# Optimization experiments

Hardware: AMD Instinct MI355X
Metric: run time of the kernel (lower is better)

## Reference

```python
import jax, jax.numpy as jnp
import numpy as np

B, T, E, H = 4, 1024, 1024, 16
D = E // H  # head_dim = 64


def setup_inputs() -> dict:
    key = jax.random.key(0)
    ks = jax.random.split(key, 6)
    s = 0.02  # realistic init scale for stable softmax
    return {
        "hidden_states": jax.random.normal(ks[0], (B, T, E), jnp.float32),
        "attention_mask": jnp.zeros((B, 1, T, T), jnp.float32),
        "Wq": jax.random.normal(ks[1], (E, E), jnp.float32) * s,
        "bq": jnp.zeros((E,), jnp.float32),
        "Wk": jax.random.normal(ks[2], (E, E), jnp.float32) * s,
        "bk": jnp.zeros((E,), jnp.float32),
        "Wv": jax.random.normal(ks[3], (E, E), jnp.float32) * s,
        "bv": jnp.zeros((E,), jnp.float32),
        "Wo": jax.random.normal(ks[4], (E, E), jnp.float32) * s,
        "bo": jnp.zeros((E,), jnp.float32),
    }


def reference(hidden_states, attention_mask, Wq, bq, Wk, bk, Wv, bv, Wo, bo):
    b, t, e = hidden_states.shape
    scaling = jnp.asarray(D, hidden_states.dtype) ** -0.5
    # q_proj weights/bias are pre-scaled in the module; equivalent to scaling q output
    q = (hidden_states @ Wq.T + bq) * scaling      # [B,T,E]
    k = hidden_states @ Wk.T + bk                   # self-attention path (no cache)
    v = hidden_states @ Wv.T + bv
    q = q.reshape(b, t, H, D)
    k = k.reshape(b, t, H, D)
    v = v.reshape(b, t, H, D)
    # bmm(q, k^T): [B,H,T,S] score matrix (materialized, as in the original)
    scores = jnp.einsum("bthd,bshd->bhts", q, k) + attention_mask
    probs = jax.nn.softmax(scores, axis=-1)
    ctx = jnp.einsum("bhts,bshd->bthd", probs, v).reshape(b, t, e)
    return ctx @ Wo.T + bo
```

## Files before the change

### kernel.cpp

```cpp
#include <hip/hip_runtime.h>
#include <math.h>

#define BB 4
#define TT 1024
#define EE 1024
#define HH 16
#define DD 64
#define KDIM 1024
#define N_HS (4096 * 1024)
#define N_W  (1024 * 1024)
#define NQKV (BB * HH * TT * DD)
#define LOG2E 1.44269504088896340736f

typedef _Float16 f16x8 __attribute__((ext_vector_type(8)));
typedef _Float16 f16x4 __attribute__((ext_vector_type(4)));
typedef _Float16 f16x2 __attribute__((ext_vector_type(2)));
typedef float    f32x4 __attribute__((ext_vector_type(4)));

__device__ __forceinline__ unsigned short f2h(float x) {
    _Float16 h = (_Float16)x;
    return __builtin_bit_cast(unsigned short, h);
}
__device__ __forceinline__ void split_h(float x, unsigned short& hi, unsigned short& lo) {
    _Float16 h = (_Float16)x;
    hi = __builtin_bit_cast(unsigned short, h);
    lo = f2h(x - (float)h);
}

__device__ __forceinline__ f16x2 cvt_pk(float a, float b) {
    return __builtin_bit_cast(f16x2, __builtin_amdgcn_cvt_pkrtz(a, b));
}

__device__ __forceinline__ void gload16(const void* g, void* l) {
    __builtin_amdgcn_global_load_lds(
        (const __attribute__((address_space(1))) void*)g,
        (__attribute__((address_space(3))) void*)l, 16, 0, 0);
}

__device__ __forceinline__ float mx3(float a, float b, float c) {
    return fmaxf(fmaxf(a, b), c);
}

__global__ __launch_bounds__(256)
void split_kernel(const float* __restrict__ hs,
                  const float* __restrict__ Wq, const float* __restrict__ Wk,
                  const float* __restrict__ Wv, const float* __restrict__ Wo,
                  const float* __restrict__ mask, int* __restrict__ mflag,
                  unsigned short* __restrict__ ws)
{
    const int u = blockIdx.x * 256 + threadIdx.x;
    if (u < (N_HS / 4) + N_W) {
        const float* src;
        unsigned short* dst;
        if (u < (N_HS / 4)) {
            src = hs + (size_t)u * 4;
            dst = ws + (size_t)u * 4;
        } else {
            int v = u - N_HS / 4;
            int wsel = v >> 18;
            int wo   = v & 0x3FFFF;
            const float* Wsrc = (wsel == 0) ? Wq : (wsel == 1) ? Wk : (wsel == 2) ? Wv : Wo;
            src = Wsrc + (size_t)wo * 4;
            dst = ws + (size_t)N_HS + (size_t)wsel * N_W + (size_t)wo * 4;
        }
        float4 x = *(const float4*)src;
        ushort4 h4;
        h4.x = f2h(x.x); h4.y = f2h(x.y); h4.z = f2h(x.z); h4.w = f2h(x.w);
        *(ushort4*)dst = h4;
    } else {
        int v = u - ((N_HS / 4) + N_W);
        float4 x = *(const float4*)(mask + (size_t)v * 4);
        bool nz = (x.x != 0.f) || (x.y != 0.f) || (x.z != 0.f) || (x.w != 0.f);
        if (__any(nz) && (threadIdx.x & 63) == 0)
            atomicOr(mflag, 1);
    }
}

__global__ __launch_bounds__(256)
void qkv_kernel(const unsigned short* __restrict__ hsp,
                const unsigned short* __restrict__ wqp,
                const float* __restrict__ bq, const float* __restrict__ bk,
                const float* __restrict__ bv,
                unsigned short* __restrict__ qkvb)
{
    __shared__ unsigned short Ah[128 * 64], Bh[128 * 64];

    const int widx  = blockIdx.x >> 3;
    const int nbase = (blockIdx.x & 7) * 128;
    const int mbase = blockIdx.y * 128;
    const unsigned short* Wp = wqp + (size_t)widx * N_W;
    const float* bias = (widx == 0) ? bq : (widx == 1) ? bk : bv;
    unsigned short* dst = qkvb + (size_t)widx * NQKV;
    const float scale = (widx == 0) ? 0.125f * LOG2E : 1.0f;

    const int tid  = threadIdx.x;
    const int w    = tid >> 6;
    const int lane = tid & 63;
    const int quad = lane >> 4;
    const int l16  = lane & 15;
    const int wm   = (w >> 1) * 64;
    const int wn   = (w & 1) * 64;

    f32x4 acc[4][4];
#pragma unroll
    for (int i = 0; i < 4; i++)
#pragma unroll
        for (int j = 0; j < 4; j++) acc[i][j] = (f32x4)0.f;

#pragma unroll 1
    for (int kt = 0; kt < KDIM; kt += 64) {
        __syncthreads();
#pragma unroll
        for (int i = 0; i < 4; i++) {
            int u = tid + i * 256;
            int r = u >> 3, cp = u & 7;
            int c = cp ^ (r & 7);
            gload16(hsp + (size_t)(mbase + r) * KDIM + kt + c * 8, &Ah[u * 8]);
            gload16(Wp  + (size_t)(nbase + r) * KDIM + kt + c * 8, &Bh[u * 8]);
        }
        __syncthreads();

#pragma unroll
        for (int ks = 0; ks < 2; ks++) {
            f16x8 af[4], bfr[4];
#pragma unroll
            for (int i = 0; i < 4; i++) {
                int r = wm + i * 16 + l16;
                af[i] = *(const f16x8*)&Ah[(r * 8 + ((ks * 4 + quad) ^ (r & 7))) * 8];
            }
#pragma unroll
            for (int j = 0; j < 4; j++) {
                int r = wn + j * 16 + l16;
                bfr[j] = *(const f16x8*)&Bh[(r * 8 + ((ks * 4 + quad) ^ (r & 7))) * 8];
            }
#pragma unroll
            for (int i = 0; i < 4; i++)
#pragma unroll
                for (int j = 0; j < 4; j++)
                    acc[i][j] = __builtin_amdgcn_mfma_f32_16x16x32_f16(af[i], bfr[j], acc[i][j], 0, 0, 0);
        }
    }

#pragma unroll
    for (int j = 0; j < 4; j++) {
        int n = nbase + wn + j * 16 + l16;
        int h = n >> 6, d = n & 63;
        float bj = bias[n];
#pragma unroll
        for (int i = 0; i < 4; i++)
#pragma unroll
            for (int rr = 0; rr < 4; rr++) {
                int m = mbase + wm + i * 16 + quad * 4 + rr;
                int b = m >> 10, t = m & 1023;
                dst[(((size_t)(b * HH + h) * TT + t) * DD + d)] =
                    f2h((acc[i][j][rr] + bj) * scale);
            }
    }
}

__global__ __launch_bounds__(256)
void vtrans_kernel(const unsigned short* __restrict__ vp,
                   unsigned short* __restrict__ vtp)
{
    __shared__ unsigned short Ts[64 * 72];
    const int bh = blockIdx.y;
    const int t0 = blockIdx.x * 64;
    const unsigned short* src = vp  + (size_t)bh * TT * DD + (size_t)t0 * DD;
    unsigned short*       dst = vtp + (size_t)bh * DD * TT + t0;
    const int tid = threadIdx.x;

#pragma unroll
    for (int i = 0; i < 2; i++) {
        int id = tid + i * 256;
        int r = id >> 3, c = id & 7;
        *(uint4*)&Ts[r * 72 + c * 8] = *(const uint4*)(src + (size_t)r * DD + c * 8);
    }
    __syncthreads();
#pragma unroll
    for (int i = 0; i < 2; i++) {
        int id = tid + i * 256;
        int d = id >> 3, c = id & 7;
        unsigned short tmp[8];
#pragma unroll
        for (int j = 0; j < 8; j++) tmp[j] = Ts[(c * 8 + j) * 72 + d];
        uint4 o;
        o.x = (unsigned int)tmp[0] | ((unsigned int)tmp[1] << 16);
        o.y = (unsigned int)tmp[2] | ((unsigned int)tmp[3] << 16);
        o.z = (unsigned int)tmp[4] | ((unsigned int)tmp[5] << 16);
        o.w = (unsigned int)tmp[6] | ((unsigned int)tmp[7] << 16);
        *(uint4*)(dst + (size_t)d * TT + c * 8) = o;
    }
}

__global__ __launch_bounds__(256)
void outproj_kernel(const unsigned short* __restrict__ ctxh,
                    const unsigned short* __restrict__ ctxl,
                    const unsigned short* __restrict__ wop,
                    const float* __restrict__ bo, float* __restrict__ out)
{
    __shared__ unsigned short Ach[64 * 64], Acl[64 * 64], Bh[128 * 64];

    const int nbase = blockIdx.x * 128;
    const int mbase = blockIdx.y * 64;

    const int tid  = threadIdx.x;
    const int w    = tid >> 6;
    const int lane = tid & 63;
    const int quad = lane >> 4;
    const int l16  = lane & 15;
    const int wm   = (w >> 1) * 32;
    const int wn   = (w & 1) * 64;

    f32x4 acc[2][4];
#pragma unroll
    for (int i = 0; i < 2; i++)
#pragma unroll
        for (int j = 0; j < 4; j++) acc[i][j] = (f32x4)0.f;

#pragma unroll 1
    for (int kt = 0; kt < KDIM; kt += 64) {
        __syncthreads();
#pragma unroll
        for (int i = 0; i < 2; i++) {
            int u = tid + i * 256;
            int r = u >> 3, cp = u & 7;
            int c = cp ^ (r & 7);
            size_t ga = (size_t)(mbase + r) * KDIM + kt + c * 8;
            gload16(ctxh + ga, &Ach[u * 8]);
            gload16(ctxl + ga, &Acl[u * 8]);
        }
#pragma unroll
        for (int i = 0; i < 4; i++) {
            int u = tid + i * 256;
            int r = u >> 3, cp = u & 7;
            int c = cp ^ (r & 7);
            gload16(wop + (size_t)(nbase + r) * KDIM + kt + c * 8, &Bh[u * 8]);
        }
        __syncthreads();

#pragma unroll
        for (int ks = 0; ks < 2; ks++) {
            f16x8 ah[2], al[2], bfr[4];
#pragma unroll
            for (int i = 0; i < 2; i++) {
                int r = wm + i * 16 + l16;
                int slot = (r * 8 + ((ks * 4 + quad) ^ (r & 7))) * 8;
                ah[i] = *(const f16x8*)&Ach[slot];
                al[i] = *(const f16x8*)&Acl[slot];
            }
#pragma unroll
            for (int j = 0; j < 4; j++) {
                int r = wn + j * 16 + l16;
                bfr[j] = *(const f16x8*)&Bh[(r * 8 + ((ks * 4 + quad) ^ (r & 7))) * 8];
            }
#pragma unroll
            for (int i = 0; i < 2; i++)
#pragma unroll
                for (int j = 0; j < 4; j++) {
                    acc[i][j] = __builtin_amdgcn_mfma_f32_16x16x32_f16(ah[i], bfr[j], acc[i][j], 0, 0, 0);
                    acc[i][j] = __builtin_amdgcn_mfma_f32_16x16x32_f16(al[i], bfr[j], acc[i][j], 0, 0, 0);
                }
        }
    }

#pragma unroll
    for (int j = 0; j < 4; j++) {
        int n = nbase + wn + j * 16 + l16;
        float bj = bo[n];
#pragma unroll
        for (int i = 0; i < 2; i++)
#pragma unroll
            for (int rr = 0; rr < 4; rr++) {
                int m = mbase + wm + i * 16 + quad * 4 + rr;
                out[(size_t)m * EE + n] = acc[i][j][rr] + bj;
            }
    }
}

__global__ __launch_bounds__(256)
void attn_kernel(const unsigned short* __restrict__ qp_, const unsigned short* __restrict__ kp_,
                 const unsigned short* __restrict__ vtp_,
                 const float* __restrict__ mask, const int* __restrict__ mflag,
                 unsigned short* __restrict__ ctxh, unsigned short* __restrict__ ctxl)
{
    __shared__ unsigned short Ks[2][64 * 64];
    __shared__ unsigned short Vt[2][64 * 64];

    const int orig = blockIdx.x;
    const int wgid = (orig & 7) * 64 + (orig >> 3);
    const int bh = wgid >> 3;
    const int b  = bh >> 4;
    const int h  = bh & 15;
    const int m0 = (wgid & 7) * 128;
    const size_t hoff = (size_t)bh * TT * DD;
    const unsigned short* qhp = qp_ + hoff;
    const unsigned short* khp = kp_ + hoff;
    const unsigned short* vtp = vtp_ + hoff;
    const float* mb = mask + (size_t)b * TT * TT;

    const int tid  = threadIdx.x;
    const int w    = tid >> 6;
    const int lane = tid & 63;
    const int quad = lane >> 4;
    const int l16  = lane & 15;
    const int mw   = m0 + w * 32;

    const int usemask = mflag[0];

    const int lm7 = l16 & 7;
    const int x0  = l16 * 64 + ((quad)     ^ lm7) * 8;
    const int x1  = l16 * 64 + ((4 + quad) ^ lm7) * 8;
    const int qh  = quad >> 1, ql = quad & 1;
    int yy[4];
#pragma unroll
    for (int t = 0; t < 4; t++)
        yy[t] = l16 * 64 + ((2 * t + qh) ^ lm7) * 8 + ql * 4;
    const unsigned short* Ksf = &Ks[0][0];
    const unsigned short* Vtf = &Vt[0][0];

    f16x8 qf[2][2];
#pragma unroll
    for (int g = 0; g < 2; g++)
#pragma unroll
        for (int s = 0; s < 2; s++)
            qf[g][s] = *(const f16x8*)(qhp + (size_t)(mw + g * 16 + l16) * DD + s * 32 + quad * 8);

    f32x4 o2[2][4];
#pragma unroll
    for (int g = 0; g < 2; g++)
#pragma unroll
        for (int u = 0; u < 4; u++) o2[g][u] = (f32x4)0.f;
    f32x4 lv[2];
    lv[0] = (f32x4)0.f; lv[1] = (f32x4)0.f;
    const f32x4 zc = (f32x4)0.f;
    f16x4 onesv;
    onesv[0] = (_Float16)1.f; onesv[1] = (_Float16)1.f;
    onesv[2] = (_Float16)1.f; onesv[3] = (_Float16)1.f;
    float m_i[2] = { -INFINITY, -INFINITY };

#pragma unroll
    for (int i = 0; i < 2; i++) {
        int u = tid + i * 256;
        int r = u >> 3, cp = u & 7;
        int c = cp ^ (r & 7);
        gload16(khp + (size_t)r * DD + c * 8, &Ks[0][u * 8]);
        gload16(vtp + (size_t)r * TT + c * 8, &Vt[0][u * 8]);
    }
    __syncthreads();

#pragma unroll 2
    for (int it = 0; it < 16; ++it) {
        const int n0  = it * 64;
        const int cur = it & 1;

        if (it < 15) {
#pragma unroll
            for (int i = 0; i < 2; i++) {
                int u = tid + i * 256;
                int r = u >> 3, cp = u & 7;
                int c = cp ^ (r & 7);
                gload16(khp + (size_t)(n0 + 64 + r) * DD + c * 8, &Ks[cur ^ 1][u * 8]);
                gload16(vtp + (size_t)r * TT + n0 + 64 + c * 8,   &Vt[cur ^ 1][u * 8]);
            }
        }

        f32x4 st[2][4];
        if (usemask) {
#pragma unroll
            for (int g = 0; g < 2; g++)
#pragma unroll
                for (int t = 0; t < 4; t++)
#pragma unroll
                    for (int r = 0; r < 4; r++)
                        st[g][t][r] = mb[(size_t)(mw + g * 16 + l16) * TT + n0 + 16 * t + quad * 4 + r] * LOG2E;
        } else {
#pragma unroll
            for (int g = 0; g < 2; g++)
#pragma unroll
                for (int t = 0; t < 4; t++) st[g][t] = zc;
        }

        __builtin_amdgcn_s_setprio(1);
#pragma unroll
        for (int t = 0; t < 4; t++) {
            const f16x8 kf = *(const f16x8*)(Ksf + cur * 4096 + x0 + t * 1024);
            st[0][t] = __builtin_amdgcn_mfma_f32_16x16x32_f16(kf, qf[0][0], st[0][t], 0, 0, 0);
            st[1][t] = __builtin_amdgcn_mfma_f32_16x16x32_f16(kf, qf[1][0], st[1][t], 0, 0, 0);
        }
#pragma unroll
        for (int t = 0; t < 4; t++) {
            const f16x8 kf = *(const f16x8*)(Ksf + cur * 4096 + x1 + t * 1024);
            st[0][t] = __builtin_amdgcn_mfma_f32_16x16x32_f16(kf, qf[0][1], st[0][t], 0, 0, 0);
            st[1][t] = __builtin_amdgcn_mfma_f32_16x16x32_f16(kf, qf[1][1], st[1][t], 0, 0, 0);
        }
        __builtin_amdgcn_s_setprio(0);

        f16x4 pb[2][4];
#pragma unroll
        for (int g = 0; g < 2; g++) {
            float g0 = mx3(st[g][0][0], st[g][0][1], st[g][0][2]);
            float g1 = mx3(st[g][0][3], st[g][1][0], st[g][1][1]);
            float g2 = mx3(st[g][1][2], st[g][1][3], st[g][2][0]);
            float g3 = mx3(st[g][2][1], st[g][2][2], st[g][2][3]);
            float g4 = mx3(st[g][3][0], st[g][3][1], st[g][3][2]);
            float rm = fmaxf(mx3(g0, g1, g2), mx3(g3, g4, st[g][3][3]));
            rm = fmaxf(rm, __shfl_xor(rm, 16));
            rm = fmaxf(rm, __shfl_xor(rm, 32));

            if (__any(rm > m_i[g] + 8.f)) {
                float mn    = fmaxf(m_i[g], rm);
                float alpha = exp2f(m_i[g] - mn);
                m_i[g] = mn;
#pragma unroll
                for (int rr = 0; rr < 4; rr++) lv[g][rr] *= alpha;
#pragma unroll
                for (int u = 0; u < 4; u++)
#pragma unroll
                    for (int rr = 0; rr < 4; rr++) o2[g][u][rr] *= alpha;
            }

#pragma unroll
            for (int t = 0; t < 4; t++) {
                float p0 = exp2f(st[g][t][0] - m_i[g]);
                float p1 = exp2f(st[g][t][1] - m_i[g]);
                float p2 = exp2f(st[g][t][2] - m_i[g]);
                float p3 = exp2f(st[g][t][3] - m_i[g]);
                f16x2 plo = cvt_pk(p0, p1);
                f16x2 phi = cvt_pk(p2, p3);
                f16x4 pv;
                pv[0] = plo[0]; pv[1] = plo[1]; pv[2] = phi[0]; pv[3] = phi[1];
                pb[g][t] = pv;
            }
        }

        __builtin_amdgcn_s_setprio(1);
#pragma unroll
        for (int t = 0; t < 4; t++) {
            lv[0] = __builtin_amdgcn_mfma_f32_16x16x16f16(onesv, pb[0][t], lv[0], 0, 0, 0);
            lv[1] = __builtin_amdgcn_mfma_f32_16x16x16f16(onesv, pb[1][t], lv[1], 0, 0, 0);
        }
#pragma unroll
        for (int u = 0; u < 4; u++) {
#pragma unroll
            for (int t = 0; t < 4; t++) {
                const f16x4 vv = *(const f16x4*)(Vtf + cur * 4096 + yy[t] + u * 1024);
                o2[0][u] = __builtin_amdgcn_mfma_f32_16x16x16f16(vv, pb[0][t], o2[0][u], 0, 0, 0);
                o2[1][u] = __builtin_amdgcn_mfma_f32_16x16x16f16(vv, pb[1][t], o2[1][u], 0, 0, 0);
            }
        }
        __builtin_amdgcn_s_setprio(0);

        __syncthreads();
    }

#pragma unroll
    for (int g = 0; g < 2; g++) {
        float inv = 1.0f / lv[g][0];
        int m = mw + g * 16 + l16;
#pragma unroll
        for (int u = 0; u < 4; u++)
#pragma unroll
            for (int rr = 0; rr < 4; rr++) {
                float val = o2[g][u][rr] * inv;
                unsigned short hi, lo;
                split_h(val, hi, lo);
                size_t off = ((size_t)(b * TT + m)) * EE + h * DD + u * 16 + quad * 4 + rr;
                ctxh[off] = hi;
                ctxl[off] = lo;
            }
    }
}

extern "C" void kernel_launch(void* const* d_in, const int* in_sizes, int n_in,
                              void* d_out, int out_size, void* d_ws, size_t ws_size,
                              hipStream_t stream)
{
    const float* hs   = (const float*)d_in[0];
    const float* mask = (const float*)d_in[1];
    const float* Wq   = (const float*)d_in[2];
    const float* bq   = (const float*)d_in[3];
    const float* Wk   = (const float*)d_in[4];
    const float* bk   = (const float*)d_in[5];
    const float* Wv   = (const float*)d_in[6];
    const float* bv   = (const float*)d_in[7];
    const float* Wo   = (const float*)d_in[8];
    const float* bo   = (const float*)d_in[9];
    float* out = (float*)d_out;

    unsigned short* ws   = (unsigned short*)d_ws;
    unsigned short* hsp  = ws;
    unsigned short* wqp  = ws + (size_t)N_HS;
    unsigned short* wop  = wqp + 3 * (size_t)N_W;
    unsigned short* qkvb = wqp + 4 * (size_t)N_W;
    unsigned short* qp   = qkvb;
    unsigned short* kp   = qp + (size_t)NQKV;
    unsigned short* vp   = kp + (size_t)NQKV;
    unsigned short* ctxh = ws;
    unsigned short* ctxl = qkvb + 3 * (size_t)NQKV;
    unsigned short* vtp  = ctxl + (size_t)N_HS;
    int*            mflag = (int*)(vtp + (size_t)NQKV);

    (void)hipMemsetAsync(mflag, 0, sizeof(int), stream);
    split_kernel<<<12288, 256, 0, stream>>>(hs, Wq, Wk, Wv, Wo, mask, mflag, ws);
    qkv_kernel<<<dim3(24, 32), 256, 0, stream>>>(hsp, wqp, bq, bk, bv, qkvb);
    vtrans_kernel<<<dim3(TT / 64, BB * HH), 256, 0, stream>>>(vp, vtp);
    attn_kernel<<<512, 256, 0, stream>>>(qp, kp, vtp, mask, mflag, ctxh, ctxl);
    outproj_kernel<<<dim3(8, 64), 256, 0, stream>>>(ctxh, ctxl, wop, bo, out);
}
```

Before: 216.0 us.

## Double-buffer LDS tiles in QKV and output-projection GEMMs with K=32 steps

Both projection GEMMs now keep two shared-memory tile buffers, each 32 wide in K, and issue the next tile's global-to-LDS loads before computing on the current one. This hides load latency behind MFMA work and drops one barrier per iteration. The XOR swizzle is redone for the 4-chunk row layout. In exchange there are twice as many loop iterations and barriers, each with half as much MFMA work, and the overlap only helps if gload16 is truly asynchronous.

```diff
diff --git a/kernel.cpp b/kernel.cpp
--- a/kernel.cpp
+++ b/kernel.cpp
@@ -83,7 +83,7 @@
                 const float* __restrict__ bv,
                 unsigned short* __restrict__ qkvb)
 {
-    __shared__ unsigned short Ah[128 * 64], Bh[128 * 64];
+    __shared__ unsigned short Ah[2][128 * 32], Bh[2][128 * 32];
 
     const int widx  = blockIdx.x >> 3;
     const int nbase = (blockIdx.x & 7) * 128;
@@ -107,38 +107,50 @@
 #pragma unroll
         for (int j = 0; j < 4; j++) acc[i][j] = (f32x4)0.f;
 
-#pragma unroll 1
-    for (int kt = 0; kt < KDIM; kt += 64) {
+#pragma unroll
+    for (int i = 0; i < 2; i++) {
+        int u = tid + i * 256;
+        int r = u >> 2, c = u & 3;
+        int q = c ^ ((r >> 1) & 3);
+        gload16(hsp + (size_t)(mbase + r) * KDIM + q * 8, &Ah[0][u * 8]);
+        gload16(Wp  + (size_t)(nbase + r) * KDIM + q * 8, &Bh[0][u * 8]);
+    }
+    __syncthreads();
+
+#pragma unroll 2
+    for (int step = 0; step < 32; ++step) {
+        const int cur = step & 1;
+        const int kt  = step * 32;
+
+        if (step < 31) {
+#pragma unroll
+            for (int i = 0; i < 2; i++) {
+                int u = tid + i * 256;
+                int r = u >> 2, c = u & 3;
+                int q = c ^ ((r >> 1) & 3);
+                gload16(hsp + (size_t)(mbase + r) * KDIM + kt + 32 + q * 8, &Ah[cur ^ 1][u * 8]);
+                gload16(Wp  + (size_t)(nbase + r) * KDIM + kt + 32 + q * 8, &Bh[cur ^ 1][u * 8]);
+            }
+        }
+
+        f16x8 af[4], bfr[4];
+#pragma unroll
+        for (int i = 0; i < 4; i++) {
+            int r = wm + i * 16 + l16;
+            af[i] = *(const f16x8*)&Ah[cur][(r * 4 + (quad ^ ((r >> 1) & 3))) * 8];
+        }
+#pragma unroll
+        for (int j = 0; j < 4; j++) {
+            int r = wn + j * 16 + l16;
+            bfr[j] = *(const f16x8*)&Bh[cur][(r * 4 + (quad ^ ((r >> 1) & 3))) * 8];
+        }
+#pragma unroll
+        for (int i = 0; i < 4; i++)
+#pragma unroll
+            for (int j = 0; j < 4; j++)
+                acc[i][j] = __builtin_amdgcn_mfma_f32_16x16x32_f16(af[i], bfr[j], acc[i][j], 0, 0, 0);
+
         __syncthreads();
-#pragma unroll
-        for (int i = 0; i < 4; i++) {
-            int u = tid + i * 256;
-            int r = u >> 3, cp = u & 7;
-            int c = cp ^ (r & 7);
-            gload16(hsp + (size_t)(mbase + r) * KDIM + kt + c * 8, &Ah[u * 8]);
-            gload16(Wp  + (size_t)(nbase + r) * KDIM + kt + c * 8, &Bh[u * 8]);
-        }
-        __syncthreads();
-
-#pragma unroll
-        for (int ks = 0; ks < 2; ks++) {
-            f16x8 af[4], bfr[4];
-#pragma unroll
-            for (int i = 0; i < 4; i++) {
-                int r = wm + i * 16 + l16;
-                af[i] = *(const f16x8*)&Ah[(r * 8 + ((ks * 4 + quad) ^ (r & 7))) * 8];
-            }
-#pragma unroll
-            for (int j = 0; j < 4; j++) {
-                int r = wn + j * 16 + l16;
-                bfr[j] = *(const f16x8*)&Bh[(r * 8 + ((ks * 4 + quad) ^ (r & 7))) * 8];
-            }
-#pragma unroll
-            for (int i = 0; i < 4; i++)
-#pragma unroll
-                for (int j = 0; j < 4; j++)
-                    acc[i][j] = __builtin_amdgcn_mfma_f32_16x16x32_f16(af[i], bfr[j], acc[i][j], 0, 0, 0);
-        }
     }
 
 #pragma unroll
@@ -198,7 +210,7 @@
                     const unsigned short* __restrict__ wop,
                     const float* __restrict__ bo, float* __restrict__ out)
 {
-    __shared__ unsigned short Ach[64 * 64], Acl[64 * 64], Bh[128 * 64];
+    __shared__ unsigned short Ach[2][64 * 32], Acl[2][64 * 32], Bh[2][128 * 32];
 
     const int nbase = blockIdx.x * 128;
     const int mbase = blockIdx.y * 64;
@@ -217,50 +229,66 @@
 #pragma unroll
         for (int j = 0; j < 4; j++) acc[i][j] = (f32x4)0.f;
 
-#pragma unroll 1
-    for (int kt = 0; kt < KDIM; kt += 64) {
+    {
+        int r = tid >> 2, c = tid & 3;
+        int q = c ^ ((r >> 1) & 3);
+        size_t ga = (size_t)(mbase + r) * KDIM + q * 8;
+        gload16(ctxh + ga, &Ach[0][tid * 8]);
+        gload16(ctxl + ga, &Acl[0][tid * 8]);
+    }
+#pragma unroll
+    for (int i = 0; i < 2; i++) {
+        int u = tid + i * 256;
+        int r = u >> 2, c = u & 3;
+        int q = c ^ ((r >> 1) & 3);
+        gload16(wop + (size_t)(nbase + r) * KDIM + q * 8, &Bh[0][u * 8]);
+    }
+    __syncthreads();
+
+#pragma unroll 2
+    for (int step = 0; step < 32; ++step) {
+        const int cur = step & 1;
+        const int kt  = step * 32;
+
+        if (step < 31) {
+            {
+                int r = tid >> 2, c = tid & 3;
+                int q = c ^ ((r >> 1) & 3);
+                size_t ga = (size_t)(mbase + r) * KDIM + kt + 32 + q * 8;
+                gload16(ctxh + ga, &Ach[cur ^ 1][tid * 8]);
+                gload16(ctxl + ga, &Acl[cur ^ 1][tid * 8]);
+            }
+#pragma unroll
+            for (int i = 0; i < 2; i++) {
+                int u = tid + i * 256;
+                int r = u >> 2, c = u & 3;
+                int q = c ^ ((r >> 1) & 3);
+                gload16(wop + (size_t)(nbase + r) * KDIM + kt + 32 + q * 8, &Bh[cur ^ 1][u * 8]);
+            }
+        }
+
+        f16x8 ah[2], al[2], bfr[4];
+#pragma unroll
+        for (int i = 0; i < 2; i++) {
+            int r = wm + i * 16 + l16;
+            int slot = (r * 4 + (quad ^ ((r >> 1) & 3))) * 8;
+            ah[i] = *(const f16x8*)&Ach[cur][slot];
+            al[i] = *(const f16x8*)&Acl[cur][slot];
+        }
+#pragma unroll
+        for (int j = 0; j < 4; j++) {
+            int r = wn + j * 16 + l16;
+            bfr[j] = *(const f16x8*)&Bh[cur][(r * 4 + (quad ^ ((r >> 1) & 3))) * 8];
+        }
+#pragma unroll
+        for (int i = 0; i < 2; i++)
+#pragma unroll
+            for (int j = 0; j < 4; j++) {
+                acc[i][j] = __builtin_amdgcn_mfma_f32_16x16x32_f16(ah[i], bfr[j], acc[i][j], 0, 0, 0);
+                acc[i][j] = __builtin_amdgcn_mfma_f32_16x16x32_f16(al[i], bfr[j], acc[i][j], 0, 0, 0);
+            }
+
         __syncthreads();
-#pragma unroll
-        for (int i = 0; i < 2; i++) {
-            int u = tid + i * 256;
-            int r = u >> 3, cp = u & 7;
-            int c = cp ^ (r & 7);
-            size_t ga = (size_t)(mbase + r) * KDIM + kt + c * 8;
-            gload16(ctxh + ga, &Ach[u * 8]);
-            gload16(ctxl + ga, &Acl[u * 8]);
-        }
-#pragma unroll
-        for (int i = 0; i < 4; i++) {
-            int u = tid + i * 256;
-            int r = u >> 3, cp = u & 7;
-            int c = cp ^ (r & 7);
-            gload16(wop + (size_t)(nbase + r) * KDIM + kt + c * 8, &Bh[u * 8]);
-        }
-        __syncthreads();
-
-#pragma unroll
-        for (int ks = 0; ks < 2; ks++) {
-            f16x8 ah[2], al[2], bfr[4];
-#pragma unroll
-            for (int i = 0; i < 2; i++) {
-                int r = wm + i * 16 + l16;
-                int slot = (r * 8 + ((ks * 4 + quad) ^ (r & 7))) * 8;
-                ah[i] = *(const f16x8*)&Ach[slot];
-                al[i] = *(const f16x8*)&Acl[slot];
-            }
-#pragma unroll
-            for (int j = 0; j < 4; j++) {
-                int r = wn + j * 16 + l16;
-                bfr[j] = *(const f16x8*)&Bh[(r * 8 + ((ks * 4 + quad) ^ (r & 7))) * 8];
-            }
-#pragma unroll
-            for (int i = 0; i < 2; i++)
-#pragma unroll
-                for (int j = 0; j < 4; j++) {
-                    acc[i][j] = __builtin_amdgcn_mfma_f32_16x16x32_f16(ah[i], bfr[j], acc[i][j], 0, 0, 0);
-                    acc[i][j] = __builtin_amdgcn_mfma_f32_16x16x32_f16(al[i], bfr[j], acc[i][j], 0, 0, 0);
-                }
-        }
     }
 
 #pragma unroll
```

Measured after the change: 219.4 us. Within noise of the previous version (+1.6%).
